# Optimization experiments

Hardware: AMD Instinct MI355X
Metric: run time of the kernel (lower is better)

Reference implementation:

```python
import jax, jax.numpy as jnp
import numpy as np

H = 256      # hidden_size
B = 32       # batch
T = 4096     # timesteps / graph nodes
E = 8192     # edges per graph
PATH = 1
EXPAND_WEIGHT = 0.1
MODE = 'son'


def setup_inputs() -> dict:
    key = jax.random.key(0)
    ks = jax.random.split(key, 6)
    hidden = jax.random.normal(ks[0], (B, H), jnp.float32)
    encoder_outputs = jax.random.normal(ks[1], (T, B, H), jnp.float32)
    edges_src = jax.random.randint(ks[2], (B, E), 0, T)
    edges_dst = jax.random.randint(ks[3], (B, E), 0, T)
    # nn.Linear(2H, 2H) params (kaiming-uniform-ish scale) and the v vector
    lim = 1.0 / np.sqrt(2 * H)
    W_attn = jax.random.uniform(ks[4], (2 * H, 2 * H), jnp.float32, -lim, lim)
    b_attn = jnp.zeros((2 * H,), jnp.float32)
    v = jax.random.uniform(ks[5], (2 * H,), jnp.float32, -lim, lim)
    return {"hidden": hidden, "encoder_outputs": encoder_outputs,
            "edges_src": edges_src, "edges_dst": edges_dst,
            "W_attn": W_attn, "b_attn": b_attn, "v": v}


def reference(hidden, encoder_outputs, edges_src, edges_dst, W_attn, b_attn, v):
    Bb, Hh = hidden.shape
    Tt = encoder_outputs.shape[0]
    # h: [B, T, H] (hidden repeated over timesteps); enc: [B, T, H]
    h = jnp.broadcast_to(hidden[:, None, :], (Bb, Tt, Hh))
    enc = jnp.transpose(encoder_outputs, (1, 0, 2))
    # score: tanh(Linear(cat)) then v . energy -> [B, T]
    energy = jnp.tanh(jnp.concatenate([h, enc], axis=2) @ W_attn.T + b_attn)
    scores = jnp.einsum('btd,d->bt', energy, v)
    w = jax.nn.softmax(scores, axis=1)
    # expand_attn: scatter-add along graph edges, skipping consecutive (y == x+1)
    mask = (edges_dst != edges_src + 1).astype(w.dtype)  # [B, E]
    def scatter(wb, src, dst, m):
        if MODE == 'son':
            return jnp.zeros_like(wb).at[dst].add(wb[src] * m)
        else:
            return jnp.zeros_like(wb).at[src].add(wb[dst] * m)
    for _ in range(PATH):
        w = jax.vmap(scatter)(w, edges_src, edges_dst, mask) * EXPAND_WEIGHT
    return w[:, None, :]  # [B, 1, T]
```

## Files before the change

### kernel.cpp

```cpp
#include <hip/hip_runtime.h>
#include <hip/hip_bf16.h>

typedef __attribute__((ext_vector_type(8))) short bf16x8;
typedef __attribute__((ext_vector_type(4))) float f32x4;

#define HD 256
#define NB 32
#define NT 4096
#define NE 8192
#define N2 512

static __device__ __forceinline__ unsigned short f2bf(float f) {
  unsigned int u = __float_as_uint(f);
  u += 0x7fff + ((u >> 16) & 1);
  return (unsigned short)(u >> 16);
}
static __device__ __forceinline__ short4 cvt4(float4 a) {
  return make_short4((short)f2bf(a.x), (short)f2bf(a.y),
                     (short)f2bf(a.z), (short)f2bf(a.w));
}
static __device__ __forceinline__ float fast_tanh(float x) {
  float e = __builtin_amdgcn_exp2f(x * 2.8853900817779268f);
  return __builtin_fmaf(-2.f, __builtin_amdgcn_rcpf(e + 1.f), 1.f);
}
static __device__ __forceinline__ bf16x8 pack8(float4 a, float4 b) {
  union { bf16x8 v; unsigned int u[4]; } r;
  r.u[0] = (__float_as_uint(a.y) & 0xffff0000u) | (__float_as_uint(a.x) >> 16);
  r.u[1] = (__float_as_uint(a.w) & 0xffff0000u) | (__float_as_uint(a.z) >> 16);
  r.u[2] = (__float_as_uint(b.y) & 0xffff0000u) | (__float_as_uint(b.x) >> 16);
  r.u[3] = (__float_as_uint(b.w) & 0xffff0000u) | (__float_as_uint(b.z) >> 16);
  return r.v;
}

__global__ __launch_bounds__(256) void prep(
    const float* __restrict__ hidden, const float* __restrict__ Wattn,
    const float* __restrict__ battn, float* __restrict__ cvecT,
    short* __restrict__ Wbf) {
  const int tid = threadIdx.x;
  if (blockIdx.x < 256) {
    __shared__ float Ws[64 * 260];
    __shared__ float Hs[HD];
    const int chunk = blockIdx.x & 7;
    const int b = blockIdx.x >> 3;
#pragma unroll
    for (int it = 0; it < 16; ++it) {
      int f = it * 1024 + tid * 4;
      int i = f >> 8, k = f & 255;
      float4 w4 = *(const float4*)(Wattn + (chunk * 64 + i) * N2 + k);
      *(float4*)&Ws[i * 260 + k] = w4;
    }
    if (tid < 64)
      *(float4*)&Hs[tid * 4] = *(const float4*)(hidden + b * HD + tid * 4);
    __syncthreads();
    const int nl = tid >> 2;
    const int kb = (tid & 3) * 64;
    float sum = 0.f;
#pragma unroll
    for (int z = 0; z < 64; z += 4) {
      float4 h4 = *(const float4*)&Hs[kb + z];
      float4 w4 = *(const float4*)&Ws[nl * 260 + kb + z];
      sum = fmaf(h4.x, w4.x, sum);
      sum = fmaf(h4.y, w4.y, sum);
      sum = fmaf(h4.z, w4.z, sum);
      sum = fmaf(h4.w, w4.w, sum);
    }
    sum += __shfl_xor(sum, 1, 64);
    sum += __shfl_xor(sum, 2, 64);
    if ((tid & 3) == 0)
      cvecT[(chunk * 64 + nl) * NB + b] = sum + battn[chunk * 64 + nl];
  } else {
    int f = (blockIdx.x - 256) * 1024 + tid * 4;
    int n = f >> 8, k = f & 255;
    float4 w4 = *(const float4*)(Wattn + n * N2 + HD + k);
    *(short4*)(Wbf + f) = cvt4(w4);
  }
}

static __device__ __forceinline__ void bload(bf16x8* dst, const short* __restrict__ Wbf,
                                             int nbase, int q, int kk) {
#pragma unroll
  for (int nf = 0; nf < 4; ++nf)
    dst[nf] = *(const bf16x8*)(Wbf + (nbase + nf * 16) * HD + kk * 32 + q * 8);
}

static __device__ __forceinline__ void kstep(f32x4 acc[4][4], const short* Abf,
                                             const bf16x8* b, int m, int q, int ks) {
#pragma unroll
  for (int mi = 0; mi < 4; ++mi) {
    const int r = mi * 16 + m;
    const int cc = ks * 4 + q;
    const int slot = (cc & ~7) | ((cc & 7) ^ (r & 7));
    bf16x8 af = *(const bf16x8*)&Abf[r * 256 + slot * 8];
#pragma unroll
    for (int nf = 0; nf < 4; ++nf)
      acc[mi][nf] =
          __builtin_amdgcn_mfma_f32_16x16x32_bf16(af, b[nf], acc[mi][nf], 0, 0, 0);
  }
}

__global__ __launch_bounds__(512, 4) void score_gemm(
    const float* __restrict__ enc, const short* __restrict__ Wbf,
    const float* __restrict__ cvecT, const float* __restrict__ vvec,
    float* __restrict__ scores) {
  __shared__ short Abf[64 * 256];
  __shared__ float part[8][64];
  const int tid = threadIdx.x;
  const int w = tid >> 6, lane = tid & 63, q = lane >> 4, m = lane & 15;
  const int row0 = blockIdx.x * 64;

#pragma unroll
  for (int i = 0; i < 4; ++i) {
    const int g = i * 512 + tid;
    const int r = g >> 5, c = g & 31;
    const float* src = enc + (row0 + r) * HD + c * 8;
    float4 a0 = *(const float4*)src;
    float4 a1 = *(const float4*)(src + 4);
    const int slot = (c & ~7) | ((c & 7) ^ (r & 7));
    *(bf16x8*)&Abf[r * 256 + slot * 8] = pack8(a0, a1);
  }

  f32x4 acc[4][4];
#pragma unroll
  for (int mi = 0; mi < 4; ++mi)
#pragma unroll
    for (int nf = 0; nf < 4; ++nf) acc[mi][nf] = (f32x4){0.f, 0.f, 0.f, 0.f};

  const int nbase = w * 64 + m;
  bf16x8 b0[4], b1[4];
  bload(b0, Wbf, nbase, q, 0);

  __syncthreads();

#pragma unroll 1
  for (int ks2 = 0; ks2 < 4; ++ks2) {
    const int ks = ks2 * 2;
    bload(b1, Wbf, nbase, q, ks + 1);
    kstep(acc, Abf, b0, m, q, ks);
    if (ks2 < 3) bload(b0, Wbf, nbase, q, ks + 2);
    kstep(acc, Abf, b1, m, q, ks + 1);
  }

  float p[4][4];
#pragma unroll
  for (int mi = 0; mi < 4; ++mi)
#pragma unroll
    for (int j = 0; j < 4; ++j) p[mi][j] = 0.f;

#pragma unroll
  for (int nf = 0; nf < 4; ++nf) {
    const int n = w * 64 + nf * 16 + m;
    const float vv = vvec[n];
    const f32x4 cvA = *(const f32x4*)(cvecT + n * NB + 4 * q);
    const f32x4 cvB = *(const f32x4*)(cvecT + n * NB + 16 + 4 * q);
#pragma unroll
    for (int mi = 0; mi < 4; ++mi) {
      const f32x4 cv = (mi & 1) ? cvB : cvA;
#pragma unroll
      for (int j = 0; j < 4; ++j)
        p[mi][j] += fast_tanh(acc[mi][nf][j] + cv[j]) * vv;
    }
  }
#pragma unroll
  for (int mi = 0; mi < 4; ++mi) {
#pragma unroll
    for (int j = 0; j < 4; ++j) {
      float e = p[mi][j];
      e += __shfl_xor(e, 1, 64);
      e += __shfl_xor(e, 2, 64);
      e += __shfl_xor(e, 4, 64);
      e += __shfl_xor(e, 8, 64);
      if (m == 0) part[w][mi * 16 + 4 * q + j] = e;
    }
  }
  __syncthreads();
  if (tid < 64) {
    const int r = row0 + tid;
    float s = 0.f;
#pragma unroll
    for (int ww = 0; ww < 8; ++ww) s += part[ww][tid];
    scores[(r & 31) * NT + (r >> 5)] = s;
  }
}

__global__ __launch_bounds__(1024) void softmax_scatter(
    const float* __restrict__ sc, const int* __restrict__ esrc,
    const int* __restrict__ edst, float* __restrict__ out) {
  __shared__ float wls[NT];
  __shared__ float accs[NT];
  __shared__ float rtmp[16];
  __shared__ float rmax, rinv;
  const int b = blockIdx.x;
  const int tid = threadIdx.x;
  const int wid = tid >> 6, lane = tid & 63;

  float s[4];
  float mx = -1e30f;
#pragma unroll
  for (int p = 0; p < 4; ++p) {
    s[p] = sc[b * NT + tid + p * 1024];
    mx = fmaxf(mx, s[p]);
  }
#pragma unroll
  for (int d = 32; d >= 1; d >>= 1) mx = fmaxf(mx, __shfl_xor(mx, d, 64));
  if (lane == 0) rtmp[wid] = mx;
  __syncthreads();
  if (tid == 0) {
    float mm = rtmp[0];
#pragma unroll
    for (int i = 1; i < 16; ++i) mm = fmaxf(mm, rtmp[i]);
    rmax = mm;
  }
  __syncthreads();
  mx = rmax;
  float e[4];
  float sm = 0.f;
#pragma unroll
  for (int p = 0; p < 4; ++p) {
    e[p] = __expf(s[p] - mx);
    sm += e[p];
  }
#pragma unroll
  for (int d = 32; d >= 1; d >>= 1) sm += __shfl_xor(sm, d, 64);
  if (lane == 0) rtmp[wid] = sm;
  __syncthreads();
  if (tid == 0) {
    float tt = 0.f;
#pragma unroll
    for (int i = 0; i < 16; ++i) tt += rtmp[i];
    rinv = 0.1f / tt;
  }
  __syncthreads();
  const float inv = rinv;
#pragma unroll
  for (int p = 0; p < 4; ++p) {
    wls[tid + p * 1024] = e[p] * inv;
    accs[tid + p * 1024] = 0.f;
  }
  __syncthreads();
#pragma unroll
  for (int i = 0; i < 8; ++i) {
    const int eid = b * NE + tid + i * 1024;
    const int ss = esrc[eid];
    const int dd = edst[eid];
    const float wv = wls[ss];
    if (dd != ss + 1) atomicAdd(&accs[dd], wv);
  }
  __syncthreads();
#pragma unroll
  for (int p = 0; p < 4; ++p)
    out[b * NT + tid + p * 1024] = accs[tid + p * 1024];
}

extern "C" void kernel_launch(void* const* d_in, const int* in_sizes, int n_in,
                              void* d_out, int out_size, void* d_ws, size_t ws_size,
                              hipStream_t stream) {
  const float* hidden = (const float*)d_in[0];
  const float* enc    = (const float*)d_in[1];
  const int*   esrc   = (const int*)d_in[2];
  const int*   edst   = (const int*)d_in[3];
  const float* Wattn  = (const float*)d_in[4];
  const float* battn  = (const float*)d_in[5];
  const float* vvec   = (const float*)d_in[6];
  float* out = (float*)d_out;

  char* ws = (char*)d_ws;
  float* cvecT  = (float*)ws;
  short* Wbf    = (short*)(ws + 65536);
  float* scores = (float*)(ws + 65536 + 262144);

  prep<<<384, 256, 0, stream>>>(hidden, Wattn, battn, cvecT, Wbf);
  score_gemm<<<(NB * NT) / 64, 512, 0, stream>>>(enc, Wbf, cvecT, vvec, scores);
  softmax_scatter<<<NB, 1024, 0, stream>>>(scores, esrc, edst, out);
}
```

Before: 279.2 us.

## Double score GEMM row tile and retile bf16 weights for contiguous B loads

The score GEMM now uses 1024-thread blocks covering 128 encoder rows. Two groups of 8 waves share each block, and every wave loads the same B fragments from global memory. The bf16 weight copy is rearranged into a k-chunked [k/32][n][32] layout, so each bload reads contiguous 512-byte spans per fragment. This is meant to halve B-matrix global traffic per row and improve load coalescing. In exchange it doubles LDS use per block (64KB for A), and launch_bounds(1024,4) may be unattainable, which would raise register pressure or cut occupancy.

```diff
diff --git a/kernel.cpp b/kernel.cpp
--- a/kernel.cpp
+++ b/kernel.cpp
@@ -35,7 +35,7 @@
 __global__ __launch_bounds__(256) void prep(
     const float* __restrict__ hidden, const float* __restrict__ Wattn,
     const float* __restrict__ battn, float* __restrict__ cvecT,
-    short* __restrict__ Wbf) {
+    short* __restrict__ WbfT) {
   const int tid = threadIdx.x;
   if (blockIdx.x < 256) {
     __shared__ float Ws[64 * 260];
@@ -72,22 +72,24 @@
     int f = (blockIdx.x - 256) * 1024 + tid * 4;
     int n = f >> 8, k = f & 255;
     float4 w4 = *(const float4*)(Wattn + n * N2 + HD + k);
-    *(short4*)(Wbf + f) = cvt4(w4);
-  }
-}
-
-static __device__ __forceinline__ void bload(bf16x8* dst, const short* __restrict__ Wbf,
+    *(short4*)(WbfT + ((k >> 5) * 512 + n) * 32 + (k & 31)) = cvt4(w4);
+  }
+}
+
+static __device__ __forceinline__ void bload(bf16x8* dst, const short* __restrict__ Wp,
                                              int nbase, int q, int kk) {
+  const short* base = Wp + (kk * 512 + nbase) * 32 + q * 8;
 #pragma unroll
   for (int nf = 0; nf < 4; ++nf)
-    dst[nf] = *(const bf16x8*)(Wbf + (nbase + nf * 16) * HD + kk * 32 + q * 8);
+    dst[nf] = *(const bf16x8*)(base + nf * 16 * 32);
 }
 
 static __device__ __forceinline__ void kstep(f32x4 acc[4][4], const short* Abf,
-                                             const bf16x8* b, int m, int q, int ks) {
+                                             const bf16x8* b, int rb, int m, int q,
+                                             int ks) {
 #pragma unroll
   for (int mi = 0; mi < 4; ++mi) {
-    const int r = mi * 16 + m;
+    const int r = rb + mi * 16 + m;
     const int cc = ks * 4 + q;
     const int slot = (cc & ~7) | ((cc & 7) ^ (r & 7));
     bf16x8 af = *(const bf16x8*)&Abf[r * 256 + slot * 8];
@@ -98,20 +100,21 @@
   }
 }
 
-__global__ __launch_bounds__(512, 4) void score_gemm(
-    const float* __restrict__ enc, const short* __restrict__ Wbf,
+__global__ __launch_bounds__(1024, 4) void score_gemm(
+    const float* __restrict__ enc, const short* __restrict__ WbfT,
     const float* __restrict__ cvecT, const float* __restrict__ vvec,
     float* __restrict__ scores) {
-  __shared__ short Abf[64 * 256];
-  __shared__ float part[8][64];
+  __shared__ short Abf[128 * 256];
+  __shared__ float part[16][64];
   const int tid = threadIdx.x;
   const int w = tid >> 6, lane = tid & 63, q = lane >> 4, m = lane & 15;
-  const int row0 = blockIdx.x * 64;
+  const int g = w >> 3, wl = w & 7;
+  const int row0 = blockIdx.x * 128;
 
 #pragma unroll
   for (int i = 0; i < 4; ++i) {
-    const int g = i * 512 + tid;
-    const int r = g >> 5, c = g & 31;
+    const int gg = i * 1024 + tid;
+    const int r = gg >> 5, c = gg & 31;
     const float* src = enc + (row0 + r) * HD + c * 8;
     float4 a0 = *(const float4*)src;
     float4 a1 = *(const float4*)(src + 4);
@@ -125,19 +128,20 @@
 #pragma unroll
     for (int nf = 0; nf < 4; ++nf) acc[mi][nf] = (f32x4){0.f, 0.f, 0.f, 0.f};
 
-  const int nbase = w * 64 + m;
+  const int nbase = wl * 64 + m;
+  const int rb = g * 64;
   bf16x8 b0[4], b1[4];
-  bload(b0, Wbf, nbase, q, 0);
+  bload(b0, WbfT, nbase, q, 0);
 
   __syncthreads();
 
 #pragma unroll 1
   for (int ks2 = 0; ks2 < 4; ++ks2) {
     const int ks = ks2 * 2;
-    bload(b1, Wbf, nbase, q, ks + 1);
-    kstep(acc, Abf, b0, m, q, ks);
-    if (ks2 < 3) bload(b0, Wbf, nbase, q, ks + 2);
-    kstep(acc, Abf, b1, m, q, ks + 1);
+    bload(b1, WbfT, nbase, q, ks + 1);
+    kstep(acc, Abf, b0, rb, m, q, ks);
+    if (ks2 < 3) bload(b0, WbfT, nbase, q, ks + 2);
+    kstep(acc, Abf, b1, rb, m, q, ks + 1);
   }
 
   float p[4][4];
@@ -148,7 +152,7 @@
 
 #pragma unroll
   for (int nf = 0; nf < 4; ++nf) {
-    const int n = w * 64 + nf * 16 + m;
+    const int n = wl * 64 + nf * 16 + m;
     const float vv = vvec[n];
     const f32x4 cvA = *(const f32x4*)(cvecT + n * NB + 4 * q);
     const f32x4 cvB = *(const f32x4*)(cvecT + n * NB + 16 + 4 * q);
@@ -173,11 +177,11 @@
     }
   }
   __syncthreads();
-  if (tid < 64) {
+  if (tid < 128) {
     const int r = row0 + tid;
     float s = 0.f;
 #pragma unroll
-    for (int ww = 0; ww < 8; ++ww) s += part[ww][tid];
+    for (int ww = 0; ww < 8; ++ww) s += part[(tid >> 6) * 8 + ww][tid & 63];
     scores[(r & 31) * NT + (r >> 5)] = s;
   }
 }
@@ -265,10 +269,10 @@
 
   char* ws = (char*)d_ws;
   float* cvecT  = (float*)ws;
-  short* Wbf    = (short*)(ws + 65536);
+  short* WbfT   = (short*)(ws + 65536);
   float* scores = (float*)(ws + 65536 + 262144);
 
-  prep<<<384, 256, 0, stream>>>(hidden, Wattn, battn, cvecT, Wbf);
-  score_gemm<<<(NB * NT) / 64, 512, 0, stream>>>(enc, Wbf, cvecT, vvec, scores);
+  prep<<<384, 256, 0, stream>>>(hidden, Wattn, battn, cvecT, WbfT);
+  score_gemm<<<(NB * NT) / 128, 1024, 0, stream>>>(enc, WbfT, cvecT, vvec, scores);
   softmax_scatter<<<NB, 1024, 0, stream>>>(scores, esrc, edst, out);
 }
```

Result: no change. 274.5 us (-1.7%).

## Fuse prep, score GEMM and softmax-scatter into one cooperative persistent kernel

Applied to the files above, without the earlier changes.

Replaces the three launches with a single cooperative kernel of 256 blocks separated by grid-wide syncs. Each block computes part of the hidden projection and converts its share of the weights to a k-major bf16 layout, then loops over 8 row tiles. While the current tile's MFMA runs, it prefetches the next tile's encoder rows into registers. The softmax and edge scatter then run on 32 blocks of 512 threads. This removes launch gaps and adds software pipelining, at the cost of grid-sync overhead, fewer blocks during the GEMM phase and a serial tail where only 32 blocks work.

```diff
diff --git a/kernel.cpp b/kernel.cpp
--- a/kernel.cpp
+++ b/kernel.cpp
@@ -1,5 +1,8 @@
 #include <hip/hip_runtime.h>
 #include <hip/hip_bf16.h>
+#include <hip/hip_cooperative_groups.h>
+
+namespace cg = cooperative_groups;
 
 typedef __attribute__((ext_vector_type(8))) short bf16x8;
 typedef __attribute__((ext_vector_type(4))) float f32x4;
@@ -32,55 +35,12 @@
   return r.v;
 }
 
-__global__ __launch_bounds__(256) void prep(
-    const float* __restrict__ hidden, const float* __restrict__ Wattn,
-    const float* __restrict__ battn, float* __restrict__ cvecT,
-    short* __restrict__ Wbf) {
-  const int tid = threadIdx.x;
-  if (blockIdx.x < 256) {
-    __shared__ float Ws[64 * 260];
-    __shared__ float Hs[HD];
-    const int chunk = blockIdx.x & 7;
-    const int b = blockIdx.x >> 3;
-#pragma unroll
-    for (int it = 0; it < 16; ++it) {
-      int f = it * 1024 + tid * 4;
-      int i = f >> 8, k = f & 255;
-      float4 w4 = *(const float4*)(Wattn + (chunk * 64 + i) * N2 + k);
-      *(float4*)&Ws[i * 260 + k] = w4;
-    }
-    if (tid < 64)
-      *(float4*)&Hs[tid * 4] = *(const float4*)(hidden + b * HD + tid * 4);
-    __syncthreads();
-    const int nl = tid >> 2;
-    const int kb = (tid & 3) * 64;
-    float sum = 0.f;
-#pragma unroll
-    for (int z = 0; z < 64; z += 4) {
-      float4 h4 = *(const float4*)&Hs[kb + z];
-      float4 w4 = *(const float4*)&Ws[nl * 260 + kb + z];
-      sum = fmaf(h4.x, w4.x, sum);
-      sum = fmaf(h4.y, w4.y, sum);
-      sum = fmaf(h4.z, w4.z, sum);
-      sum = fmaf(h4.w, w4.w, sum);
-    }
-    sum += __shfl_xor(sum, 1, 64);
-    sum += __shfl_xor(sum, 2, 64);
-    if ((tid & 3) == 0)
-      cvecT[(chunk * 64 + nl) * NB + b] = sum + battn[chunk * 64 + nl];
-  } else {
-    int f = (blockIdx.x - 256) * 1024 + tid * 4;
-    int n = f >> 8, k = f & 255;
-    float4 w4 = *(const float4*)(Wattn + n * N2 + HD + k);
-    *(short4*)(Wbf + f) = cvt4(w4);
-  }
-}
-
-static __device__ __forceinline__ void bload(bf16x8* dst, const short* __restrict__ Wbf,
+static __device__ __forceinline__ void bload(bf16x8* dst, const short* __restrict__ Wp,
                                              int nbase, int q, int kk) {
+  const short* base = Wp + (kk * 512 + nbase) * 32 + q * 8;
 #pragma unroll
   for (int nf = 0; nf < 4; ++nf)
-    dst[nf] = *(const bf16x8*)(Wbf + (nbase + nf * 16) * HD + kk * 32 + q * 8);
+    dst[nf] = *(const bf16x8*)(base + nf * 16 * 32);
 }
 
 static __device__ __forceinline__ void kstep(f32x4 acc[4][4], const short* Abf,
@@ -98,157 +58,215 @@
   }
 }
 
-__global__ __launch_bounds__(512, 4) void score_gemm(
-    const float* __restrict__ enc, const short* __restrict__ Wbf,
-    const float* __restrict__ cvecT, const float* __restrict__ vvec,
-    float* __restrict__ scores) {
+__global__ __launch_bounds__(512, 2) void fused(
+    const float* __restrict__ hidden, const float* __restrict__ enc,
+    const int* __restrict__ esrc, const int* __restrict__ edst,
+    const float* __restrict__ Wattn, const float* __restrict__ battn,
+    const float* __restrict__ vvec, float* __restrict__ cvecT,
+    short* __restrict__ WbfT, float* __restrict__ scores,
+    float* __restrict__ out) {
+  cg::grid_group grid = cg::this_grid();
+  const int tid = threadIdx.x;
+  const int bx = blockIdx.x;
+
+  {
+    const int nn = tid >> 8;
+    const int n = 2 * bx + nn;
+    const int b = (tid >> 3) & 31;
+    const int s = tid & 7;
+    const float* wrow = Wattn + n * N2 + s * 32;
+    const float* hrow = hidden + b * HD + s * 32;
+    float sum = 0.f;
+#pragma unroll
+    for (int z = 0; z < 32; z += 4) {
+      float4 w4 = *(const float4*)(wrow + z);
+      float4 h4 = *(const float4*)(hrow + z);
+      sum = fmaf(h4.x, w4.x, sum);
+      sum = fmaf(h4.y, w4.y, sum);
+      sum = fmaf(h4.z, w4.z, sum);
+      sum = fmaf(h4.w, w4.w, sum);
+    }
+    sum += __shfl_xor(sum, 1, 64);
+    sum += __shfl_xor(sum, 2, 64);
+    sum += __shfl_xor(sum, 4, 64);
+    if (s == 0) cvecT[n * NB + b] = sum + battn[n];
+    if (tid < 128) {
+      const int f = bx * 128 + tid;
+      const int n2 = f >> 6, k4 = (f & 63) * 4;
+      float4 w4 = *(const float4*)(Wattn + n2 * N2 + HD + k4);
+      *(short4*)(WbfT + ((k4 >> 5) * 512 + n2) * 32 + (k4 & 31)) = cvt4(w4);
+    }
+  }
+  grid.sync();
+
   __shared__ short Abf[64 * 256];
   __shared__ float part[8][64];
-  const int tid = threadIdx.x;
   const int w = tid >> 6, lane = tid & 63, q = lane >> 4, m = lane & 15;
-  const int row0 = blockIdx.x * 64;
-
-#pragma unroll
-  for (int i = 0; i < 4; ++i) {
-    const int g = i * 512 + tid;
-    const int r = g >> 5, c = g & 31;
-    const float* src = enc + (row0 + r) * HD + c * 8;
-    float4 a0 = *(const float4*)src;
-    float4 a1 = *(const float4*)(src + 4);
-    const int slot = (c & ~7) | ((c & 7) ^ (r & 7));
-    *(bf16x8*)&Abf[r * 256 + slot * 8] = pack8(a0, a1);
-  }
-
-  f32x4 acc[4][4];
-#pragma unroll
-  for (int mi = 0; mi < 4; ++mi)
-#pragma unroll
-    for (int nf = 0; nf < 4; ++nf) acc[mi][nf] = (f32x4){0.f, 0.f, 0.f, 0.f};
-
   const int nbase = w * 64 + m;
-  bf16x8 b0[4], b1[4];
-  bload(b0, Wbf, nbase, q, 0);
-
-  __syncthreads();
-
-#pragma unroll 1
-  for (int ks2 = 0; ks2 < 4; ++ks2) {
-    const int ks = ks2 * 2;
-    bload(b1, Wbf, nbase, q, ks + 1);
-    kstep(acc, Abf, b0, m, q, ks);
-    if (ks2 < 3) bload(b0, Wbf, nbase, q, ks + 2);
-    kstep(acc, Abf, b1, m, q, ks + 1);
-  }
-
-  float p[4][4];
-#pragma unroll
-  for (int mi = 0; mi < 4; ++mi)
-#pragma unroll
-    for (int j = 0; j < 4; ++j) p[mi][j] = 0.f;
-
+
+  f32x4 cvA[4], cvB[4];
+  float vv[4];
 #pragma unroll
   for (int nf = 0; nf < 4; ++nf) {
     const int n = w * 64 + nf * 16 + m;
-    const float vv = vvec[n];
-    const f32x4 cvA = *(const f32x4*)(cvecT + n * NB + 4 * q);
-    const f32x4 cvB = *(const f32x4*)(cvecT + n * NB + 16 + 4 * q);
+    cvA[nf] = *(const f32x4*)(cvecT + n * NB + 4 * q);
+    cvB[nf] = *(const f32x4*)(cvecT + n * NB + 16 + 4 * q);
+    vv[nf] = vvec[n];
+  }
+
+  float4 pa[4], pb[4];
+  {
+    const int row0 = bx * 8 * 64;
+#pragma unroll
+    for (int i = 0; i < 4; ++i) {
+      const int gg = i * 512 + tid, r = gg >> 5, c = gg & 31;
+      const float* src = enc + (row0 + r) * HD + c * 8;
+      pa[i] = *(const float4*)src;
+      pb[i] = *(const float4*)(src + 4);
+    }
+  }
+
+#pragma unroll 1
+  for (int tt = 0; tt < 8; ++tt) {
+    const int row0 = (bx * 8 + tt) * 64;
+#pragma unroll
+    for (int i = 0; i < 4; ++i) {
+      const int gg = i * 512 + tid, r = gg >> 5, c = gg & 31;
+      const int slot = (c & ~7) | ((c & 7) ^ (r & 7));
+      *(bf16x8*)&Abf[r * 256 + slot * 8] = pack8(pa[i], pb[i]);
+    }
+    __syncthreads();
+
+    f32x4 acc[4][4];
+#pragma unroll
+    for (int mi = 0; mi < 4; ++mi)
+#pragma unroll
+      for (int nf = 0; nf < 4; ++nf) acc[mi][nf] = (f32x4){0.f, 0.f, 0.f, 0.f};
+
+    bf16x8 b0[4], b1[4];
+    bload(b0, WbfT, nbase, q, 0);
+#pragma unroll
+    for (int ks2 = 0; ks2 < 4; ++ks2) {
+      const int ks = ks2 * 2;
+      bload(b1, WbfT, nbase, q, ks + 1);
+      kstep(acc, Abf, b0, m, q, ks);
+      if (ks2 < 3) bload(b0, WbfT, nbase, q, ks + 2);
+      if (ks2 == 3 && tt < 7) {
+        const int nr0 = row0 + 64;
+#pragma unroll
+        for (int i = 0; i < 4; ++i) {
+          const int gg = i * 512 + tid, r = gg >> 5, c = gg & 31;
+          const float* src = enc + (nr0 + r) * HD + c * 8;
+          pa[i] = *(const float4*)src;
+          pb[i] = *(const float4*)(src + 4);
+        }
+      }
+      kstep(acc, Abf, b1, m, q, ks + 1);
+    }
+
+    float pr[4][4];
+#pragma unroll
+    for (int mi = 0; mi < 4; ++mi)
+#pragma unroll
+      for (int j = 0; j < 4; ++j) pr[mi][j] = 0.f;
+#pragma unroll
+    for (int nf = 0; nf < 4; ++nf) {
+#pragma unroll
+      for (int mi = 0; mi < 4; ++mi) {
+        const f32x4 cv = (mi & 1) ? cvB[nf] : cvA[nf];
+#pragma unroll
+        for (int j = 0; j < 4; ++j)
+          pr[mi][j] += fast_tanh(acc[mi][nf][j] + cv[j]) * vv[nf];
+      }
+    }
 #pragma unroll
     for (int mi = 0; mi < 4; ++mi) {
-      const f32x4 cv = (mi & 1) ? cvB : cvA;
-#pragma unroll
-      for (int j = 0; j < 4; ++j)
-        p[mi][j] += fast_tanh(acc[mi][nf][j] + cv[j]) * vv;
-    }
-  }
-#pragma unroll
-  for (int mi = 0; mi < 4; ++mi) {
-#pragma unroll
-    for (int j = 0; j < 4; ++j) {
-      float e = p[mi][j];
-      e += __shfl_xor(e, 1, 64);
-      e += __shfl_xor(e, 2, 64);
-      e += __shfl_xor(e, 4, 64);
-      e += __shfl_xor(e, 8, 64);
-      if (m == 0) part[w][mi * 16 + 4 * q + j] = e;
-    }
-  }
-  __syncthreads();
-  if (tid < 64) {
-    const int r = row0 + tid;
-    float s = 0.f;
-#pragma unroll
-    for (int ww = 0; ww < 8; ++ww) s += part[ww][tid];
-    scores[(r & 31) * NT + (r >> 5)] = s;
-  }
-}
-
-__global__ __launch_bounds__(1024) void softmax_scatter(
-    const float* __restrict__ sc, const int* __restrict__ esrc,
-    const int* __restrict__ edst, float* __restrict__ out) {
-  __shared__ float wls[NT];
-  __shared__ float accs[NT];
-  __shared__ float rtmp[16];
-  __shared__ float rmax, rinv;
-  const int b = blockIdx.x;
-  const int tid = threadIdx.x;
-  const int wid = tid >> 6, lane = tid & 63;
-
-  float s[4];
-  float mx = -1e30f;
-#pragma unroll
-  for (int p = 0; p < 4; ++p) {
-    s[p] = sc[b * NT + tid + p * 1024];
-    mx = fmaxf(mx, s[p]);
-  }
-#pragma unroll
-  for (int d = 32; d >= 1; d >>= 1) mx = fmaxf(mx, __shfl_xor(mx, d, 64));
-  if (lane == 0) rtmp[wid] = mx;
-  __syncthreads();
-  if (tid == 0) {
-    float mm = rtmp[0];
-#pragma unroll
-    for (int i = 1; i < 16; ++i) mm = fmaxf(mm, rtmp[i]);
-    rmax = mm;
-  }
-  __syncthreads();
-  mx = rmax;
-  float e[4];
-  float sm = 0.f;
-#pragma unroll
-  for (int p = 0; p < 4; ++p) {
-    e[p] = __expf(s[p] - mx);
-    sm += e[p];
-  }
-#pragma unroll
-  for (int d = 32; d >= 1; d >>= 1) sm += __shfl_xor(sm, d, 64);
-  if (lane == 0) rtmp[wid] = sm;
-  __syncthreads();
-  if (tid == 0) {
-    float tt = 0.f;
-#pragma unroll
-    for (int i = 0; i < 16; ++i) tt += rtmp[i];
-    rinv = 0.1f / tt;
-  }
-  __syncthreads();
-  const float inv = rinv;
-#pragma unroll
-  for (int p = 0; p < 4; ++p) {
-    wls[tid + p * 1024] = e[p] * inv;
-    accs[tid + p * 1024] = 0.f;
-  }
-  __syncthreads();
-#pragma unroll
-  for (int i = 0; i < 8; ++i) {
-    const int eid = b * NE + tid + i * 1024;
-    const int ss = esrc[eid];
-    const int dd = edst[eid];
-    const float wv = wls[ss];
-    if (dd != ss + 1) atomicAdd(&accs[dd], wv);
-  }
-  __syncthreads();
-#pragma unroll
-  for (int p = 0; p < 4; ++p)
-    out[b * NT + tid + p * 1024] = accs[tid + p * 1024];
+#pragma unroll
+      for (int j = 0; j < 4; ++j) {
+        float e = pr[mi][j];
+        e += __shfl_xor(e, 1, 64);
+        e += __shfl_xor(e, 2, 64);
+        e += __shfl_xor(e, 4, 64);
+        e += __shfl_xor(e, 8, 64);
+        if (m == 0) part[w][mi * 16 + 4 * q + j] = e;
+      }
+    }
+    __syncthreads();
+    if (tid < 64) {
+      const int r = row0 + tid;
+      float s = 0.f;
+#pragma unroll
+      for (int ww = 0; ww < 8; ++ww) s += part[ww][tid];
+      scores[(r & 31) * NT + (r >> 5)] = s;
+    }
+  }
+  grid.sync();
+
+  if (bx < NB) {
+    __shared__ float wls[NT];
+    __shared__ float accs[NT];
+    __shared__ float rtmp[8];
+    __shared__ float rmax, rinv;
+    const int b = bx;
+    const int wid = tid >> 6;
+
+    float s[8];
+    float mx = -1e30f;
+#pragma unroll
+    for (int p = 0; p < 8; ++p) {
+      s[p] = scores[b * NT + tid + p * 512];
+      mx = fmaxf(mx, s[p]);
+    }
+#pragma unroll
+    for (int d = 32; d >= 1; d >>= 1) mx = fmaxf(mx, __shfl_xor(mx, d, 64));
+    if ((tid & 63) == 0) rtmp[wid] = mx;
+    __syncthreads();
+    if (tid == 0) {
+      float mm = rtmp[0];
+#pragma unroll
+      for (int i = 1; i < 8; ++i) mm = fmaxf(mm, rtmp[i]);
+      rmax = mm;
+    }
+    __syncthreads();
+    mx = rmax;
+    float e[8];
+    float sm = 0.f;
+#pragma unroll
+    for (int p = 0; p < 8; ++p) {
+      e[p] = __expf(s[p] - mx);
+      sm += e[p];
+    }
+#pragma unroll
+    for (int d = 32; d >= 1; d >>= 1) sm += __shfl_xor(sm, d, 64);
+    if ((tid & 63) == 0) rtmp[wid] = sm;
+    __syncthreads();
+    if (tid == 0) {
+      float tt = 0.f;
+#pragma unroll
+      for (int i = 0; i < 8; ++i) tt += rtmp[i];
+      rinv = 0.1f / tt;
+    }
+    __syncthreads();
+    const float inv = rinv;
+#pragma unroll
+    for (int p = 0; p < 8; ++p) {
+      wls[tid + p * 512] = e[p] * inv;
+      accs[tid + p * 512] = 0.f;
+    }
+    __syncthreads();
+#pragma unroll
+    for (int i = 0; i < 16; ++i) {
+      const int eid = b * NE + tid + i * 512;
+      const int ss = esrc[eid];
+      const int dd = edst[eid];
+      const float wv = wls[ss];
+      if (dd != ss + 1) atomicAdd(&accs[dd], wv);
+    }
+    __syncthreads();
+#pragma unroll
+    for (int p = 0; p < 8; ++p)
+      out[b * NT + tid + p * 512] = accs[tid + p * 512];
+  }
 }
 
 extern "C" void kernel_launch(void* const* d_in, const int* in_sizes, int n_in,
@@ -265,10 +283,11 @@
 
   char* ws = (char*)d_ws;
   float* cvecT  = (float*)ws;
-  short* Wbf    = (short*)(ws + 65536);
+  short* WbfT   = (short*)(ws + 65536);
   float* scores = (float*)(ws + 65536 + 262144);
 
-  prep<<<384, 256, 0, stream>>>(hidden, Wattn, battn, cvecT, Wbf);
-  score_gemm<<<(NB * NT) / 64, 512, 0, stream>>>(enc, Wbf, cvecT, vvec, scores);
-  softmax_scatter<<<NB, 1024, 0, stream>>>(scores, esrc, edst, out);
-}
+  void* args[] = {&hidden, &enc, &esrc, &edst, &Wattn, &battn, &vvec,
+                  &cvecT, &WbfT, &scores, &out};
+  hipLaunchCooperativeKernel((const void*)fused, dim3(256), dim3(512), args, 0,
+                             stream);
+}
```

Result: slower. 348.8 us (+25.0%).
